# Kernel tuning notes

Measured on AMD Instinct MI355X. Metric: run time of the kernel, lower is better.

The kernel has to match this reference:

```python
import jax, jax.numpy as jnp
import numpy as np

B, T, D, H = 2, 2048, 1024, 16
NEG = -65504.0


def setup_inputs() -> dict:
    key = jax.random.key(0)
    ks = jax.random.split(key, 12)
    std = float(np.sqrt(2.0 / (D + D)))  # xavier_normal for square weights
    inp = {
        'q': jax.random.normal(ks[0], (B, T, D), jnp.float32),
        'k': jax.random.normal(ks[1], (B, T, D), jnp.float32),
        'v': jax.random.normal(ks[2], (B, T, D), jnp.float32),
        'mask': jax.random.randint(ks[3], (B, T), 0, 2, jnp.int32),
        # weights stored as (in, out) so y = x @ W + b
        'Wq': jax.random.normal(ks[4], (D, D), jnp.float32) * std,
        'bq': jnp.zeros((D,), jnp.float32),
        'Wk': jax.random.normal(ks[5], (D, D), jnp.float32) * std,
        'bk': jnp.zeros((D,), jnp.float32),
        'Wv': jax.random.normal(ks[6], (D, D), jnp.float32) * std,
        'bv': jnp.zeros((D,), jnp.float32),
        'Wo': jax.random.normal(ks[7], (D, D), jnp.float32) * std,
        'bo': jnp.zeros((D,), jnp.float32),
    }
    return inp


def reference(q, k, v, mask, Wq, bq, Wk, bk, Wv, bv, Wo, bo):
    b, t, _ = q.shape
    dim_a = Wq.shape[1]
    dh = dim_a // H
    # projections, then split into heads: (b, t, H, dh)
    qh = (q @ Wq + bq).reshape(b, t, H, dh)
    kh = (k @ Wk + bk).reshape(b, t, H, dh)
    vh = (v @ Wv + bv).reshape(b, t, H, dh)
    # NOTE: module scales by 1/sqrt(dim_a) with the FULL dim_a, not per-head
    a = jnp.einsum('bthd,bshd->bhts', qh, kh) / jnp.sqrt(jnp.float32(dim_a))
    # 2D mask broadcasts over query positions: (b, 1, 1, t_keys)
    a = jnp.where(mask[:, None, None, :] == 0, NEG, a)
    a = jax.nn.softmax(a, axis=-1)  # dropout_prob=0 (eval mode)
    o = jnp.einsum('bhts,bshd->bthd', a, vh).reshape(b, t, dim_a)
    return o @ Wo + bo
```

## Files before the change

kernel.cpp:

```cpp
#include <hip/hip_runtime.h>
#include <hip/hip_bf16.h>
#include <math.h>

#define B_ 2
#define T_ 2048
#define D_ 1024
#define H_ 16
#define QSCALE (0.03125f * 1.44269504088896f)

typedef _Float16 f16;
using f16x4 = __attribute__((ext_vector_type(4))) _Float16;
using f16x8 = __attribute__((ext_vector_type(8))) _Float16;
using f32x4 = __attribute__((ext_vector_type(4))) float;

__device__ __forceinline__ void gl16(const void* g, void* l) {
  __builtin_amdgcn_global_load_lds(
      (__attribute__((address_space(1))) void*)g,
      (__attribute__((address_space(3))) void*)l, 16, 0, 0);
}

__device__ __forceinline__ unsigned lds_a32(const void* p) {
  return (unsigned)(size_t)(__attribute__((address_space(3))) const char*)p;
}

__global__ __launch_bounds__(256) void prep0(
    const int* __restrict__ mask, int* __restrict__ inv, int* __restrict__ nk) {
  __shared__ int cnt[256];
  const int b = blockIdx.x;
  const int tid = threadIdx.x;
  int loc[8];
  int c = 0;
#pragma unroll
  for (int i = 0; i < 8; ++i) {
    loc[i] = mask[b * T_ + tid * 8 + i];
    c += loc[i];
  }
  cnt[tid] = c;
  __syncthreads();
  for (int off = 1; off < 256; off <<= 1) {
    int vsh = (tid >= off) ? cnt[tid - off] : 0;
    __syncthreads();
    cnt[tid] += vsh;
    __syncthreads();
  }
  int pos = cnt[tid] - c;
#pragma unroll
  for (int i = 0; i < 8; ++i) {
    const int t = tid * 8 + i;
    inv[b * T_ + t] = loc[i] ? pos : -1;
    pos += loc[i];
  }
  if (tid == 255) nk[b] = cnt[255];
}

__global__ __launch_bounds__(256) void prep1(
    const float* __restrict__ q, const float* __restrict__ k,
    const float* __restrict__ v, const int* __restrict__ inv,
    const float* __restrict__ Wq, const float* __restrict__ Wk,
    const float* __restrict__ Wv, const float* __restrict__ Wo,
    const float* __restrict__ bq, const float* __restrict__ bk,
    const float* __restrict__ bv, const float* __restrict__ bo,
    f16* __restrict__ xqkv, f16* __restrict__ Wt, float* __restrict__ bias) {
  __shared__ float sh[64][65];
  const int bid = blockIdx.x;
  const int tid = threadIdx.x;

  if (bid < 6144) {
    const int z = bid / 2048;
    const float* src = (z == 0) ? q : (z == 1) ? k : v;
    const size_t i = ((size_t)(bid % 2048) * 256 + tid) * 8;
    float4 a = *(const float4*)(src + i);
    float4 b4 = *(const float4*)(src + i + 4);
    f16x8 o;
    o[0] = (f16)a.x;  o[1] = (f16)a.y;  o[2] = (f16)a.z;  o[3] = (f16)a.w;
    o[4] = (f16)b4.x; o[5] = (f16)b4.y; o[6] = (f16)b4.z; o[7] = (f16)b4.w;
    if (z == 0) {
      *(f16x8*)(xqkv + i) = o;
    } else {
      const int tl = (int)(i >> 10);
      const int bb = tl >> 11, t = tl & 2047;
      const int j = inv[bb * T_ + t];
      if (j >= 0)
        *(f16x8*)(xqkv + (size_t)z * 4194304 +
                  (((size_t)(bb * T_ + j)) << 10) + (i & 1023)) = o;
    }
  } else if (bid < 7168) {
    const int id = bid - 6144;
    const int z = id >> 8;
    const int k0 = ((id >> 4) & 15) * 64, n0 = (id & 15) * 64;
    const float* W = (z == 0) ? Wq : (z == 1) ? Wk : (z == 2) ? Wv : Wo;
    const int r = tid >> 2, c0 = (tid & 3) * 16;
#pragma unroll
    for (int i = 0; i < 4; ++i)
      *(float4*)&sh[r][c0 + 4 * i] =
          *(const float4*)&W[(size_t)(k0 + r) * 1024 + n0 + c0 + 4 * i];
    __syncthreads();
    f16 tmp[16];
#pragma unroll
    for (int i = 0; i < 16; ++i) tmp[i] = (f16)sh[c0 + i][r];
    f16* dst = Wt + (size_t)z * 1048576 + (size_t)(n0 + r) * 1024 + k0 + c0;
    *(f16x8*)dst = *(f16x8*)&tmp[0];
    *(f16x8*)(dst + 8) = *(f16x8*)&tmp[8];
  } else {
    const int i = (bid - 7168) * 256 + tid;
    const int z = i >> 10;
    const float* s = (z == 0) ? bq : (z == 1) ? bk : (z == 2) ? bv : bo;
    bias[i] = s[i & 1023];
  }
}

__global__ __launch_bounds__(256, 4) void gemm_r2(
    const f16* __restrict__ Xb, const f16* __restrict__ Wtb,
    const float* __restrict__ biasb, void* __restrict__ C0,
    void* __restrict__ C1, void* __restrict__ C2,
    const int* __restrict__ nkd, float qscale) {
  __shared__ __align__(16) char lds[32768];
  const int z = blockIdx.z;
  const int m0 = blockIdx.y * 128, n0 = blockIdx.x * 128;

  if (z) {
    const int nb = nkd[m0 >> 11];
    const int lim = ((nb + 63) >> 6) << 6;
    if ((m0 & 2047) >= lim) return;
  }

  const f16* X  = Xb  + (size_t)z * (4096 * 1024);
  const f16* Wt = Wtb + (size_t)z * (1024 * 1024);
  const float* bias = biasb + (size_t)z * 1024;
  f16* C = (f16*)((z == 0) ? C0 : (z == 1) ? C1 : C2);
  const float scl = (z == 0) ? qscale : 1.f;

  const int tid = threadIdx.x;
  const int wave = tid >> 6, lane = tid & 63;
  const int quad = lane >> 4, l16 = lane & 15;
  const int wm = wave & 1, wn = wave >> 1;

  const int r0 = tid >> 2;
  const int ssw = (tid & 3) ^ ((r0 >> 1) & 3);
  const f16* ap0 = X  + (size_t)(m0 + r0) * 1024 + ssw * 8;
  const f16* ap1 = ap0 + (size_t)64 * 1024;
  const f16* bp0 = Wt + (size_t)(n0 + r0) * 1024 + ssw * 8;
  const f16* bp1 = bp0 + (size_t)64 * 1024;
  char* al = lds + tid * 16;
  char* bl = lds + 8192 + tid * 16;

  const int sw16 = 16 * (quad ^ ((l16 >> 1) & 3));
  const unsigned a32 = lds_a32(lds + (64 * wm + l16) * 64 + sw16);
  const unsigned b32 = lds_a32(lds + 8192 + (64 * wn + l16) * 64 + sw16);

  f32x4 acc[4][4] = {};

#define R2_ISSUE(tt, sl) do {                                               \
    gl16(ap0 + (tt) * 32, al + (sl) * 16384);                               \
    gl16(ap1 + (tt) * 32, al + (sl) * 16384 + 4096);                        \
    gl16(bp0 + (tt) * 32, bl + (sl) * 16384);                               \
    gl16(bp1 + (tt) * 32, bl + (sl) * 16384 + 4096);                        \
    __builtin_amdgcn_sched_barrier(0);                                      \
  } while (0)

#define R2_WAIT(n) do {                                                     \
    asm volatile("s_waitcnt vmcnt(" #n ")");                                \
    __builtin_amdgcn_sched_barrier(0);                                      \
  } while (0)

#define R2_BAR() do {                                                       \
    __builtin_amdgcn_sched_barrier(0);                                      \
    asm volatile("s_barrier");                                              \
    __builtin_amdgcn_sched_barrier(0);                                      \
  } while (0)

#define R2_STR_(x) #x
#define R2_STR(x) R2_STR_(x)
#define DSR(dst, base, OFF)                                                 \
  asm volatile("ds_read_b128 %0, %1 offset:" R2_STR(OFF)                    \
               : "=v"(dst) : "v"(base))

#define R2_COMPUTE(sl) do {                                                 \
    R2_BAR();                                                               \
    const unsigned aa = a32 + (sl) * 16384;                                 \
    const unsigned bb = b32 + (sl) * 16384;                                 \
    f16x8 af[4], bf[4];                                                     \
    DSR(af[0], aa, 0);    DSR(af[1], aa, 1024);                             \
    DSR(bf[0], bb, 0);    DSR(bf[1], bb, 1024);                             \
    DSR(bf[2], bb, 2048); DSR(bf[3], bb, 3072);                             \
    DSR(af[2], aa, 2048); DSR(af[3], aa, 3072);                             \
    asm volatile("s_waitcnt lgkmcnt(2)");                                   \
    __builtin_amdgcn_sched_barrier(0);                                      \
    __builtin_amdgcn_s_setprio(1);                                          \
    _Pragma("unroll")                                                       \
    for (int mi = 0; mi < 2; ++mi)                                          \
      _Pragma("unroll")                                                     \
      for (int ni = 0; ni < 4; ++ni)                                        \
        acc[mi][ni] = __builtin_amdgcn_mfma_f32_16x16x32_f16(               \
            af[mi], bf[ni], acc[mi][ni], 0, 0, 0);                          \
    asm volatile("s_waitcnt lgkmcnt(0)");                                   \
    __builtin_amdgcn_sched_barrier(0);                                      \
    _Pragma("unroll")                                                       \
    for (int mi = 2; mi < 4; ++mi)                                          \
      _Pragma("unroll")                                                     \
      for (int ni = 0; ni < 4; ++ni)                                        \
        acc[mi][ni] = __builtin_amdgcn_mfma_f32_16x16x32_f16(               \
            af[mi], bf[ni], acc[mi][ni], 0, 0, 0);                          \
    __builtin_amdgcn_s_setprio(0);                                          \
    R2_BAR();                                                               \
  } while (0)

  R2_ISSUE(0, 0);
  for (int j = 0; j < 15; ++j) {
    R2_ISSUE(2 * j + 1, 1); R2_WAIT(4); R2_COMPUTE(0);
    R2_ISSUE(2 * j + 2, 0); R2_WAIT(4); R2_COMPUTE(1);
  }
  R2_ISSUE(31, 1); R2_WAIT(4); R2_COMPUTE(0);
  R2_WAIT(0); R2_COMPUTE(1);

#undef R2_ISSUE
#undef R2_WAIT
#undef R2_BAR
#undef DSR
#undef R2_STR
#undef R2_STR_
#undef R2_COMPUTE

  const int cm = m0 + 64 * wm + 4 * quad;
  const int cn = n0 + 64 * wn + l16;
  float bv[4];
#pragma unroll
  for (int ni = 0; ni < 4; ++ni) bv[ni] = bias[cn + 16 * ni];

  if (z == 0) {
#pragma unroll
    for (int mi = 0; mi < 4; ++mi)
#pragma unroll
      for (int r = 0; r < 4; ++r) {
        f16* row = C + (size_t)(cm + 16 * mi + r) * 1024;
#pragma unroll
        for (int ni = 0; ni < 4; ++ni)
          row[cn + 16 * ni] = (f16)((acc[mi][ni][r] + bv[ni]) * scl);
      }
  } else {
    const int nb = nkd[m0 >> 11];
#pragma unroll
    for (int mi = 0; mi < 4; ++mi)
#pragma unroll
      for (int r = 0; r < 4; ++r) {
        const int m = cm + 16 * mi + r;
        const bool ok = (m & 2047) < nb;
        f16* row = C + (size_t)m * 1024;
#pragma unroll
        for (int ni = 0; ni < 4; ++ni)
          row[cn + 16 * ni] = ok ? (f16)(acc[mi][ni][r] + bv[ni]) : (f16)0.f;
      }
  }
}

template <int TM, typename OT>
__global__ __launch_bounds__(256) void gemm_bt(
    const f16* __restrict__ Xb, const f16* __restrict__ Wtb,
    const float* __restrict__ biasb, void* __restrict__ C0,
    const int* __restrict__ unused, int M, int N, int K, float qscale) {
  constexpr int FM = TM / 32;
  __shared__ __align__(16) f16 As[TM * 32];
  __shared__ __align__(16) f16 Bs[128 * 32];
  const f16* X  = Xb;
  const f16* Wt = Wtb;
  const float* bias = biasb;
  OT* C = (OT*)C0;
  const float scl = qscale;

  const int tid = threadIdx.x;
  const int wave = tid >> 6, lane = tid & 63;
  const int quad = lane >> 4, l16 = lane & 15;
  const int wm = wave & 1, wn = wave >> 1;
  const int m0 = blockIdx.y * TM, n0 = blockIdx.x * 128;

  f32x4 acc[FM][4] = {};

  const f16* asrc = X  + (size_t)(m0 + (tid >> 2)) * K + (tid & 3) * 8;
  const f16* bsrc = Wt + (size_t)(n0 + (tid >> 2)) * K + (tid & 3) * 8;
  char* aldst = (char*)As + tid * 16;
  char* bldst = (char*)Bs + tid * 16;
  const size_t rstep = (size_t)64 * K;

  const int NK = K >> 5;
  for (int kt = 0; kt < NK; ++kt) {
    if (kt) __syncthreads();
    gl16(asrc, aldst);
    if constexpr (TM == 128) gl16(asrc + rstep, aldst + 4096);
    gl16(bsrc, bldst);
    gl16(bsrc + rstep, bldst + 4096);
    asrc += 32; bsrc += 32;
    __syncthreads();

    f16x8 af[FM], bf[4];
#pragma unroll
    for (int t = 0; t < FM; ++t)
      af[t] = *(const f16x8*)&As[((TM / 2) * wm + 16 * t + l16) * 32 + quad * 8];
#pragma unroll
    for (int t = 0; t < 4; ++t)
      bf[t] = *(const f16x8*)&Bs[(64 * wn + 16 * t + l16) * 32 + quad * 8];
#pragma unroll
    for (int i = 0; i < FM; ++i)
#pragma unroll
      for (int j = 0; j < 4; ++j)
        acc[i][j] = __builtin_amdgcn_mfma_f32_16x16x32_f16(af[i], bf[j], acc[i][j], 0, 0, 0);
  }

  const int cm = m0 + (TM / 2) * wm + 4 * quad;
  const int cn = n0 + 64 * wn + l16;
  float bv[4];
#pragma unroll
  for (int tn = 0; tn < 4; ++tn) bv[tn] = bias[cn + 16 * tn];

#pragma unroll
  for (int tm = 0; tm < FM; ++tm)
#pragma unroll
    for (int r = 0; r < 4; ++r) {
      OT* row = C + (size_t)(cm + 16 * tm + r) * N;
#pragma unroll
      for (int tn = 0; tn < 4; ++tn)
        row[cn + 16 * tn] = (OT)((acc[tm][tn][r] + bv[tn]) * scl);
    }
}

__global__ __launch_bounds__(256) void vtrans(
    const f16* __restrict__ vhc, const int* __restrict__ nk,
    f16* __restrict__ vhT) {
  const int tt = blockIdx.x, bh = blockIdx.y;
  const int b = bh >> 4, h = bh & 15;
  const int n = nk[b];
  const int nkt = (n + 63) >> 6;
  if (tt >= nkt) return;
  __shared__ f16 t[64][72];
  const int tid = threadIdx.x;
  const int r = tid >> 2, cq = 16 * (tid & 3);

  const int j = tt * 64 + r;
  uint4 v0 = {0u, 0u, 0u, 0u}, v1 = {0u, 0u, 0u, 0u};
  if (j < n) {
    const uint4* src = (const uint4*)(vhc + ((size_t)b * T_ + j) * D_ + h * 64 + cq);
    v0 = src[0]; v1 = src[1];
  }
  *(uint4*)&t[r][cq]     = v0;
  *(uint4*)&t[r][cq + 8] = v1;
  __syncthreads();

  f16 tmp[16];
#pragma unroll
  for (int xx = 0; xx < 16; ++xx) {
    int x = (xx + r) & 15;
    tmp[x] = t[cq + x][r];
  }
  f16* dst = vhT + ((size_t)bh * 64 + r) * T_ + tt * 64 + cq;
  *(uint4*)&dst[0] = *(uint4*)&tmp[0];
  *(uint4*)&dst[8] = *(uint4*)&tmp[8];
}

__global__ __launch_bounds__(512) void attn_mfma(
    const f16* __restrict__ qh, const f16* __restrict__ khc,
    const f16* __restrict__ vhT, const int* __restrict__ nkd,
    f16* __restrict__ oat) {
  __shared__ f16 Ks[64][72];
  __shared__ f16 Vt[64][72];
  __shared__ f16 Ps[8][16][72];

  const int qt = blockIdx.x, bh = blockIdx.y;
  const int b = bh >> 4, h = bh & 15;
  const int tid = threadIdx.x;
  const int wave = tid >> 6, lane = tid & 63;
  const int quad = lane >> 4, l16 = lane & 15;
  const int sr = tid >> 3, sq = 8 * (tid & 7);

  const int n = nkd[b];
  const int nkt = (n + 63) >> 6;
  const int npad = (nkt << 6) - n;

  f16x8 qf[2];
  {
    const f16* qp = qh + ((size_t)(b * T_ + qt * 128 + wave * 16 + l16)) * D_ + h * 64 + quad * 8;
    qf[0] = *(const f16x8*)qp;
    qf[1] = *(const f16x8*)(qp + 32);
  }

  float lsum = 0.f;
  f32x4 o[4] = {};

  const f16* kbase = khc + (size_t)b * T_ * D_ + h * 64;
  const f16* vbase = vhT + ((size_t)bh * 64 + sr) * T_;

  uint4 kr, vr;
  auto load_kv = [&](int kt) {
    kr = *(const uint4*)(kbase + (size_t)(kt * 64 + sr) * D_ + sq);
    vr = *(const uint4*)(vbase + kt * 64 + sq);
  };
  if (nkt > 0) load_kv(0);

  for (int kt = 0; kt < nkt; ++kt) {
    *(uint4*)&Ks[sr][sq] = kr;
    *(uint4*)&Vt[sr][sq] = vr;
    __syncthreads();
    if (kt + 1 < nkt) load_kv(kt + 1);

#pragma unroll
    for (int tn = 0; tn < 4; ++tn) {
      f16x8 kf0 = *(const f16x8*)&Ks[16 * tn + l16][quad * 8];
      f16x8 kf1 = *(const f16x8*)&Ks[16 * tn + l16][32 + quad * 8];
      f32x4 s = {0.f, 0.f, 0.f, 0.f};
      s = __builtin_amdgcn_mfma_f32_16x16x32_f16(kf0, qf[0], s, 0, 0, 0);
      s = __builtin_amdgcn_mfma_f32_16x16x32_f16(kf1, qf[1], s, 0, 0, 0);
      float p0 = exp2f(s[0]), p1 = exp2f(s[1]);
      float p2 = exp2f(s[2]), p3 = exp2f(s[3]);
      lsum += (p0 + p1) + (p2 + p3);
      f16x4 pk;
      pk[0] = (f16)p0; pk[1] = (f16)p1; pk[2] = (f16)p2; pk[3] = (f16)p3;
      *(f16x4*)&Ps[wave][l16][16 * tn + 4 * quad] = pk;
    }

    f16x8 pf0 = *(const f16x8*)&Ps[wave][l16][quad * 8];
    f16x8 pf1 = *(const f16x8*)&Ps[wave][l16][32 + quad * 8];
#pragma unroll
    for (int t = 0; t < 4; ++t) {
      f16x8 vf0 = *(const f16x8*)&Vt[16 * t + l16][quad * 8];
      f16x8 vf1 = *(const f16x8*)&Vt[16 * t + l16][32 + quad * 8];
      o[t] = __builtin_amdgcn_mfma_f32_16x16x32_f16(pf0, vf0, o[t], 0, 0, 0);
      o[t] = __builtin_amdgcn_mfma_f32_16x16x32_f16(pf1, vf1, o[t], 0, 0, 0);
    }
    __syncthreads();
  }

  {
    float ls = lsum;
    ls += __shfl_xor(ls, 16);
    ls += __shfl_xor(ls, 32);
    ls -= (float)npad;
    const size_t orow = (size_t)(b * T_ + qt * 128 + wave * 16 + 4 * quad);
#pragma unroll
    for (int r = 0; r < 4; ++r) {
      const float iv = 1.f / __shfl(ls, 4 * quad + r);
#pragma unroll
      for (int t = 0; t < 4; ++t)
        oat[(orow + r) * D_ + h * 64 + 16 * t + l16] = (f16)(o[t][r] * iv);
    }
  }
}

extern "C" void kernel_launch(void* const* d_in, const int* in_sizes, int n_in,
                              void* d_out, int out_size, void* d_ws, size_t ws_size,
                              hipStream_t stream) {
  const float* q  = (const float*)d_in[0];
  const float* k  = (const float*)d_in[1];
  const float* v  = (const float*)d_in[2];
  const int* mask = (const int*)d_in[3];
  const float* Wq = (const float*)d_in[4];
  const float* bq = (const float*)d_in[5];
  const float* Wk = (const float*)d_in[6];
  const float* bk = (const float*)d_in[7];
  const float* Wv = (const float*)d_in[8];
  const float* bv = (const float*)d_in[9];
  const float* Wo = (const float*)d_in[10];
  const float* bo = (const float*)d_in[11];
  float* out = (float*)d_out;

  char* ws = (char*)d_ws;
  f16* xqkv  = (f16*)(ws);
  f16* Wt    = (f16*)(ws + 25165824);
  f16* qh    = (f16*)(ws + 33554432);
  f16* vhc   = (f16*)(ws + 41943040);
  f16* khc   = (f16*)(ws + 50331648);
  float* bsw = (float*)(ws + 58720256);
  int* inv   = (int*)(ws + 58736640);
  int* nk    = (int*)(ws + 58753024);
  f16* vhT   = (f16*)(ws);
  f16* oat   = (f16*)(ws + 8388608);

  const int M = B_ * T_;
  dim3 blk(256);

  prep0<<<dim3(2), blk, 0, stream>>>(mask, inv, nk);

  prep1<<<dim3(7184), blk, 0, stream>>>(q, k, v, inv, Wq, Wk, Wv, Wo,
                                        bq, bk, bv, bo, xqkv, Wt, bsw);

  gemm_r2<<<dim3(8, 32, 3), blk, 0, stream>>>(
      xqkv, Wt, bsw, qh, khc, vhc, nk, QSCALE);

  vtrans<<<dim3(32, 32), blk, 0, stream>>>(vhc, nk, vhT);

  attn_mfma<<<dim3(16, 32), dim3(512), 0, stream>>>(qh, khc, vhT, nk, oat);

  gemm_bt<64, float><<<dim3(8, 64, 1), blk, 0, stream>>>(
      oat, Wt + 3145728, bsw + 3072, out, nullptr, M, D_, D_, 1.f);
}
```

Baseline: 224.0 us.

## Deepen GEMM LDS pipeline to four stages and reuse it for output projection

The QKV projection GEMM goes from a 2-stage to a 4-stage global-to-LDS prefetch pipeline, with 64KB of LDS and three tiles kept in flight, to hide more memory latency. The kernel is templated on output type and a compaction flag. The output projection now uses this pipelined 128x128 kernel in place of the simple single-buffered gemm_bt with 64-row tiles. The larger LDS footprint may lower occupancy, since 4 blocks per CU at 64KB may not fit, and the output GEMM launches half as many blocks.

```diff
diff --git a/kernel.cpp b/kernel.cpp
--- a/kernel.cpp
+++ b/kernel.cpp
@@ -109,16 +109,17 @@
   }
 }
 
-__global__ __launch_bounds__(256, 4) void gemm_r2(
+template <typename OT, bool CMP>
+__global__ __launch_bounds__(256, 4) void gemm_r4(
     const f16* __restrict__ Xb, const f16* __restrict__ Wtb,
     const float* __restrict__ biasb, void* __restrict__ C0,
     void* __restrict__ C1, void* __restrict__ C2,
     const int* __restrict__ nkd, float qscale) {
-  __shared__ __align__(16) char lds[32768];
+  __shared__ __align__(16) char lds[65536];
   const int z = blockIdx.z;
   const int m0 = blockIdx.y * 128, n0 = blockIdx.x * 128;
 
-  if (z) {
+  if (CMP && z) {
     const int nb = nkd[m0 >> 11];
     const int lim = ((nb + 63) >> 6) << 6;
     if ((m0 & 2047) >= lim) return;
@@ -127,7 +128,7 @@
   const f16* X  = Xb  + (size_t)z * (4096 * 1024);
   const f16* Wt = Wtb + (size_t)z * (1024 * 1024);
   const float* bias = biasb + (size_t)z * 1024;
-  f16* C = (f16*)((z == 0) ? C0 : (z == 1) ? C1 : C2);
+  OT* C = (OT*)((z == 0) ? C0 : (z == 1) ? C1 : C2);
   const float scl = (z == 0) ? qscale : 1.f;
 
   const int tid = threadIdx.x;
@@ -150,7 +151,7 @@
 
   f32x4 acc[4][4] = {};
 
-#define R2_ISSUE(tt, sl) do {                                               \
+#define R4_ISSUE(tt, sl) do {                                               \
     gl16(ap0 + (tt) * 32, al + (sl) * 16384);                               \
     gl16(ap1 + (tt) * 32, al + (sl) * 16384 + 4096);                        \
     gl16(bp0 + (tt) * 32, bl + (sl) * 16384);                               \
@@ -158,25 +159,25 @@
     __builtin_amdgcn_sched_barrier(0);                                      \
   } while (0)
 
-#define R2_WAIT(n) do {                                                     \
+#define R4_WAIT(n) do {                                                     \
     asm volatile("s_waitcnt vmcnt(" #n ")");                                \
     __builtin_amdgcn_sched_barrier(0);                                      \
   } while (0)
 
-#define R2_BAR() do {                                                       \
+#define R4_BAR() do {                                                       \
     __builtin_amdgcn_sched_barrier(0);                                      \
     asm volatile("s_barrier");                                              \
     __builtin_amdgcn_sched_barrier(0);                                      \
   } while (0)
 
-#define R2_STR_(x) #x
-#define R2_STR(x) R2_STR_(x)
+#define R4_STR_(x) #x
+#define R4_STR(x) R4_STR_(x)
 #define DSR(dst, base, OFF)                                                 \
-  asm volatile("ds_read_b128 %0, %1 offset:" R2_STR(OFF)                    \
+  asm volatile("ds_read_b128 %0, %1 offset:" R4_STR(OFF)                    \
                : "=v"(dst) : "v"(base))
 
-#define R2_COMPUTE(sl) do {                                                 \
-    R2_BAR();                                                               \
+#define R4_COMPUTE(sl) do {                                                 \
+    R4_BAR();                                                               \
     const unsigned aa = a32 + (sl) * 16384;                                 \
     const unsigned bb = b32 + (sl) * 16384;                                 \
     f16x8 af[4], bf[4];                                                     \
@@ -202,24 +203,30 @@
         acc[mi][ni] = __builtin_amdgcn_mfma_f32_16x16x32_f16(               \
             af[mi], bf[ni], acc[mi][ni], 0, 0, 0);                          \
     __builtin_amdgcn_s_setprio(0);                                          \
-    R2_BAR();                                                               \
+    R4_BAR();                                                               \
   } while (0)
 
-  R2_ISSUE(0, 0);
-  for (int j = 0; j < 15; ++j) {
-    R2_ISSUE(2 * j + 1, 1); R2_WAIT(4); R2_COMPUTE(0);
-    R2_ISSUE(2 * j + 2, 0); R2_WAIT(4); R2_COMPUTE(1);
-  }
-  R2_ISSUE(31, 1); R2_WAIT(4); R2_COMPUTE(0);
-  R2_WAIT(0); R2_COMPUTE(1);
-
-#undef R2_ISSUE
-#undef R2_WAIT
-#undef R2_BAR
+  R4_ISSUE(0, 0); R4_ISSUE(1, 1); R4_ISSUE(2, 2);
+
+  for (int j = 0; j < 7; ++j) {
+    const int t4 = j * 4;
+    R4_ISSUE(t4 + 3, 3); R4_WAIT(12); R4_COMPUTE(0);
+    R4_ISSUE(t4 + 4, 0); R4_WAIT(12); R4_COMPUTE(1);
+    R4_ISSUE(t4 + 5, 1); R4_WAIT(12); R4_COMPUTE(2);
+    R4_ISSUE(t4 + 6, 2); R4_WAIT(12); R4_COMPUTE(3);
+  }
+  R4_ISSUE(31, 3); R4_WAIT(12); R4_COMPUTE(0);
+  R4_WAIT(8);  R4_COMPUTE(1);
+  R4_WAIT(4);  R4_COMPUTE(2);
+  R4_WAIT(0);  R4_COMPUTE(3);
+
+#undef R4_ISSUE
+#undef R4_WAIT
+#undef R4_BAR
 #undef DSR
-#undef R2_STR
-#undef R2_STR_
-#undef R2_COMPUTE
+#undef R4_STR
+#undef R4_STR_
+#undef R4_COMPUTE
 
   const int cm = m0 + 64 * wm + 4 * quad;
   const int cn = n0 + 64 * wn + l16;
@@ -227,15 +234,15 @@
 #pragma unroll
   for (int ni = 0; ni < 4; ++ni) bv[ni] = bias[cn + 16 * ni];
 
-  if (z == 0) {
+  if (!CMP || z == 0) {
 #pragma unroll
     for (int mi = 0; mi < 4; ++mi)
 #pragma unroll
       for (int r = 0; r < 4; ++r) {
-        f16* row = C + (size_t)(cm + 16 * mi + r) * 1024;
+        OT* row = C + (size_t)(cm + 16 * mi + r) * 1024;
 #pragma unroll
         for (int ni = 0; ni < 4; ++ni)
-          row[cn + 16 * ni] = (f16)((acc[mi][ni][r] + bv[ni]) * scl);
+          row[cn + 16 * ni] = (OT)((acc[mi][ni][r] + bv[ni]) * scl);
       }
   } else {
     const int nb = nkd[m0 >> 11];
@@ -245,81 +252,12 @@
       for (int r = 0; r < 4; ++r) {
         const int m = cm + 16 * mi + r;
         const bool ok = (m & 2047) < nb;
-        f16* row = C + (size_t)m * 1024;
+        OT* row = C + (size_t)m * 1024;
 #pragma unroll
         for (int ni = 0; ni < 4; ++ni)
-          row[cn + 16 * ni] = ok ? (f16)(acc[mi][ni][r] + bv[ni]) : (f16)0.f;
+          row[cn + 16 * ni] = ok ? (OT)(acc[mi][ni][r] + bv[ni]) : (OT)0.f;
       }
   }
-}
-
-template <int TM, typename OT>
-__global__ __launch_bounds__(256) void gemm_bt(
-    const f16* __restrict__ Xb, const f16* __restrict__ Wtb,
-    const float* __restrict__ biasb, void* __restrict__ C0,
-    const int* __restrict__ unused, int M, int N, int K, float qscale) {
-  constexpr int FM = TM / 32;
-  __shared__ __align__(16) f16 As[TM * 32];
-  __shared__ __align__(16) f16 Bs[128 * 32];
-  const f16* X  = Xb;
-  const f16* Wt = Wtb;
-  const float* bias = biasb;
-  OT* C = (OT*)C0;
-  const float scl = qscale;
-
-  const int tid = threadIdx.x;
-  const int wave = tid >> 6, lane = tid & 63;
-  const int quad = lane >> 4, l16 = lane & 15;
-  const int wm = wave & 1, wn = wave >> 1;
-  const int m0 = blockIdx.y * TM, n0 = blockIdx.x * 128;
-
-  f32x4 acc[FM][4] = {};
-
-  const f16* asrc = X  + (size_t)(m0 + (tid >> 2)) * K + (tid & 3) * 8;
-  const f16* bsrc = Wt + (size_t)(n0 + (tid >> 2)) * K + (tid & 3) * 8;
-  char* aldst = (char*)As + tid * 16;
-  char* bldst = (char*)Bs + tid * 16;
-  const size_t rstep = (size_t)64 * K;
-
-  const int NK = K >> 5;
-  for (int kt = 0; kt < NK; ++kt) {
-    if (kt) __syncthreads();
-    gl16(asrc, aldst);
-    if constexpr (TM == 128) gl16(asrc + rstep, aldst + 4096);
-    gl16(bsrc, bldst);
-    gl16(bsrc + rstep, bldst + 4096);
-    asrc += 32; bsrc += 32;
-    __syncthreads();
-
-    f16x8 af[FM], bf[4];
-#pragma unroll
-    for (int t = 0; t < FM; ++t)
-      af[t] = *(const f16x8*)&As[((TM / 2) * wm + 16 * t + l16) * 32 + quad * 8];
-#pragma unroll
-    for (int t = 0; t < 4; ++t)
-      bf[t] = *(const f16x8*)&Bs[(64 * wn + 16 * t + l16) * 32 + quad * 8];
-#pragma unroll
-    for (int i = 0; i < FM; ++i)
-#pragma unroll
-      for (int j = 0; j < 4; ++j)
-        acc[i][j] = __builtin_amdgcn_mfma_f32_16x16x32_f16(af[i], bf[j], acc[i][j], 0, 0, 0);
-  }
-
-  const int cm = m0 + (TM / 2) * wm + 4 * quad;
-  const int cn = n0 + 64 * wn + l16;
-  float bv[4];
-#pragma unroll
-  for (int tn = 0; tn < 4; ++tn) bv[tn] = bias[cn + 16 * tn];
-
-#pragma unroll
-  for (int tm = 0; tm < FM; ++tm)
-#pragma unroll
-    for (int r = 0; r < 4; ++r) {
-      OT* row = C + (size_t)(cm + 16 * tm + r) * N;
-#pragma unroll
-      for (int tn = 0; tn < 4; ++tn)
-        row[cn + 16 * tn] = (OT)((acc[tm][tn][r] + bv[tn]) * scl);
-    }
 }
 
 __global__ __launch_bounds__(256) void vtrans(
@@ -472,7 +410,6 @@
   f16* vhT   = (f16*)(ws);
   f16* oat   = (f16*)(ws + 8388608);
 
-  const int M = B_ * T_;
   dim3 blk(256);
 
   prep0<<<dim3(2), blk, 0, stream>>>(mask, inv, nk);
@@ -480,13 +417,13 @@
   prep1<<<dim3(7184), blk, 0, stream>>>(q, k, v, inv, Wq, Wk, Wv, Wo,
                                         bq, bk, bv, bo, xqkv, Wt, bsw);
 
-  gemm_r2<<<dim3(8, 32, 3), blk, 0, stream>>>(
+  gemm_r4<f16, true><<<dim3(8, 32, 3), blk, 0, stream>>>(
       xqkv, Wt, bsw, qh, khc, vhc, nk, QSCALE);
 
   vtrans<<<dim3(32, 32), blk, 0, stream>>>(vhc, nk, vhT);
 
   attn_mfma<<<dim3(16, 32), dim3(512), 0, stream>>>(qh, khc, vhT, nk, oat);
 
-  gemm_bt<64, float><<<dim3(8, 64, 1), blk, 0, stream>>>(
-      oat, Wt + 3145728, bsw + 3072, out, nullptr, M, D_, D_, 1.f);
-}
+  gemm_r4<float, false><<<dim3(8, 32, 1), blk, 0, stream>>>(
+      oat, Wt + 3145728, bsw + 3072, out, nullptr, nullptr, nullptr, 1.f);
+}
```

Measured after the change: 217.0 us. -3.1%, faster.
